# Kernel optimization log

Measured on AMD Instinct MI355X. Metric: run time of the kernel, lower is better.

Reference implementation:

```python
import jax, jax.numpy as jnp
import numpy as np

N_HEAD = 16
L_PARAM = 2  # module's L; min block = 2**L


def _build_sets(T, Lp):
    sets = []
    L = 2 ** Lp
    while L <= T:
        for i in range(T // L):
            sets.append((i * L, (i + 1) * L - 1))
        L *= 2
    return np.asarray(sets, dtype=np.int32)  # [nsets, 2]


def _get_slice(x_cum, l_idx, r_idx):
    # x_cum: [B, nh, T, hs]; returns cumulative-sum slice sums for each (l, r)
    r = x_cum[:, :, r_idx, :]
    l = x_cum[:, :, l_idx - 1, :] * (l_idx >= 1)[None, None, :, None]
    return r - l


def setup_inputs() -> dict:
    key = jax.random.key(0)
    k1, k2, k3 = jax.random.split(key, 3)
    B, T, C = 2, 2048, 1024
    x = jax.random.normal(k1, (B, T, C), dtype=jnp.float32)
    W_attn = jax.random.normal(k2, (3 * C, C), dtype=jnp.float32) * 0.02
    W_proj = jax.random.normal(k3, (C, C), dtype=jnp.float32) * 0.02
    return {"x": x, "W_attn": W_attn, "W_proj": W_proj}


def reference(x, W_attn, W_proj):
    B, T, C = x.shape
    nh, hs = N_HEAD, C // N_HEAD
    scale = 1.0 / np.sqrt(hs).astype(np.float32)

    qkv = x @ W_attn.T  # [B, T, 3C]
    q, k, v = jnp.split(qkv, 3, axis=2)
    q = q.reshape(B, T, nh, hs).transpose(0, 2, 1, 3)  # [B, nh, T, hs]
    k = k.reshape(B, T, nh, hs).transpose(0, 2, 1, 3)
    v = v.reshape(B, T, nh, hs).transpose(0, 2, 1, 3)

    # phi is identity, so q_phi = q, k_phi = k
    k_cum = jnp.cumsum(k, axis=2)
    v_cum = jnp.cumsum(v, axis=2)

    sets = _build_sets(T, L_PARAM)  # static, [nsets, 2]
    l_idx = jnp.asarray(sets[:, 0])
    r_idx = jnp.asarray(sets[:, 1])

    K = _get_slice(k_cum, l_idx, r_idx)  # [B, nh, nsets, hs]
    V = _get_slice(v_cum, l_idx, r_idx)

    t = jnp.arange(T)
    mask = t[:, None] >= r_idx[None, :]  # [T, nsets]

    att_logits = jnp.einsum('bhtd,bhsd->bhts', q, K) * scale
    att_logits = jnp.where(mask[None, None], att_logits, -jnp.inf)

    # tail term: remaining t % 2**L + 1 keys for each query
    Lmin = 2 ** L_PARAM
    tail_len = t % Lmin + 1
    l_tail = t - tail_len + 1
    K_tail = _get_slice(k_cum, l_tail, t)  # [B, nh, T, hs]
    V_tail = _get_slice(v_cum, l_tail, t)
    att_tail = jnp.sum(q * K_tail, axis=-1) * scale  # [B, nh, T]

    logits = jnp.concatenate([att_logits, att_tail[..., None]], axis=-1)
    att = jax.nn.softmax(logits, axis=-1)

    out = jnp.einsum('bhts,bhsd->bhtd', att[..., :-1], V) + att[..., -1:] * V_tail
    out = out.transpose(0, 2, 1, 3).reshape(B, T, C)
    return out @ W_proj.T
```

## Files before the change

### kernel.cpp

```cpp
#include <hip/hip_runtime.h>

typedef _Float16 f16x8 __attribute__((ext_vector_type(8)));
typedef unsigned short u16x8 __attribute__((ext_vector_type(8)));
typedef float f32x4  __attribute__((ext_vector_type(4)));
typedef unsigned short u16;

#define T_SEQ 2048
#define C_DIM 1024
#define NH 16
#define HS 64
#define S_SETS 1023
#define S_PAD 1024
#define SCALE 0.125f
#define NEG_BIG -1e30f

#define GLB(p) ((const __attribute__((address_space(1))) void*)(p))
#define LDS(p) ((__attribute__((address_space(3))) void*)(p))

__device__ __forceinline__ u16 f2h(float f) {
    _Float16 h = (_Float16)f;
    return __builtin_bit_cast(unsigned short, h);
}
__device__ __forceinline__ float h2f(u16 u) {
    _Float16 h = __builtin_bit_cast(_Float16, u);
    return (float)h;
}
__device__ __forceinline__ f32x4 mfmah(f16x8 a, f16x8 b, f32x4 c) {
    return __builtin_amdgcn_mfma_f32_16x16x32_f16(a, b, c, 0, 0, 0);
}

__global__ __launch_bounds__(256) void conv_f16(const float* __restrict__ in,
                                                u16* __restrict__ out, int n4) {
    int i = blockIdx.x * 256 + threadIdx.x;
    if (i >= n4) return;
    float4 f = ((const float4*)in)[i];
    ushort4 o;
    o.x = f2h(f.x); o.y = f2h(f.y); o.z = f2h(f.z); o.w = f2h(f.w);
    ((ushort4*)out)[i] = o;
}

__global__ __launch_bounds__(256) void gemm_qkv16(const u16* __restrict__ x16,
                                                  const u16* __restrict__ wa16,
                                                  u16* __restrict__ q16,
                                                  u16* __restrict__ k16,
                                                  u16* __restrict__ v16) {
    __shared__ u16 As[128 * 32];
    __shared__ u16 Bs[128 * 32];
    int tid = threadIdx.x, wv = tid >> 6, lane = tid & 63;
    int lm = lane & 15, quad = lane >> 4;
    int mt = blockIdx.x / 24, nt = blockIdx.x % 24;
    int wm = wv >> 1, wn = wv & 1;
    int m_off = wm * 64, n_off = wn * 64;

    const u16* gsrc;
    u16* ldst;
    int half = wv & 1;
    if (wv < 2) { gsrc = x16  + (size_t)(mt * 128 + half * 64) * C_DIM; ldst = As + half * 64 * 32; }
    else        { gsrc = wa16 + (size_t)(nt * 128 + half * 64) * C_DIM; ldst = Bs + half * 64 * 32; }
    int srow = lane >> 2, scol = (lane & 3) * 8;

    f32x4 acc[4][4];
    #pragma unroll
    for (int i = 0; i < 4; ++i)
        #pragma unroll
        for (int j = 0; j < 4; ++j) acc[i][j] = (f32x4){0.f, 0.f, 0.f, 0.f};

    for (int k0 = 0; k0 < C_DIM; k0 += 32) {
        __syncthreads();
        #pragma unroll
        for (int i = 0; i < 4; ++i) {
            int row = i * 16 + srow;
            __builtin_amdgcn_global_load_lds(
                GLB(gsrc + (size_t)row * C_DIM + k0 + scol),
                LDS(ldst + i * 512), 16, 0, 0);
        }
        __syncthreads();
        f16x8 af[4], bf[4];
        #pragma unroll
        for (int i = 0; i < 4; ++i) {
            af[i] = *(const f16x8*)(As + (m_off + i * 16 + lm) * 32 + quad * 8);
            bf[i] = *(const f16x8*)(Bs + (n_off + i * 16 + lm) * 32 + quad * 8);
        }
        #pragma unroll
        for (int mi = 0; mi < 4; ++mi)
            #pragma unroll
            for (int ni = 0; ni < 4; ++ni)
                acc[mi][ni] = mfmah(af[mi], bf[ni], acc[mi][ni]);
    }

    #pragma unroll
    for (int mi = 0; mi < 4; ++mi)
        #pragma unroll
        for (int ni = 0; ni < 4; ++ni) {
            int n = nt * 128 + n_off + ni * 16 + lm;
            int which = n >> 10, h = (n >> 6) & 15, d = n & 63;
            #pragma unroll
            for (int reg = 0; reg < 4; ++reg) {
                int m = mt * 128 + m_off + mi * 16 + quad * 4 + reg;
                int b_ = m >> 11, t = m & 2047;
                size_t oi = (((size_t)(b_ * NH + h)) * T_SEQ + t) * HS + d;
                float val = acc[mi][ni][reg];
                if (which == 0)      q16[oi] = f2h(val * SCALE);
                else if (which == 1) k16[oi] = f2h(val);
                else                 v16[oi] = f2h(val);
            }
        }
}

__global__ __launch_bounds__(256) void set_sums(const u16* __restrict__ k16,
                                                const u16* __restrict__ v16,
                                                u16* __restrict__ K16,
                                                u16* __restrict__ VT16) {
    int bh  = blockIdx.x;
    int src = blockIdx.y >> 2;
    int dc  = blockIdx.y & 3;
    int tid = threadIdx.x;
    __shared__ float lv0[512 * 16];
    __shared__ float lv1[256 * 16];
    const u16* sp = src ? v16 : k16;
    u16* op = src ? VT16 : K16;
    int dbase = dc * 16;
    for (int idx = tid; idx < 512 * 16; idx += 256) {
        int sg = idx >> 4, dd = idx & 15, d = dbase + dd;
        const u16* p = sp + ((size_t)bh * T_SEQ + sg * 4) * HS + d;
        float s = h2f(p[0]) + h2f(p[HS]) + h2f(p[2 * HS]) + h2f(p[3 * HS]);
        lv0[sg * 16 + dd] = s;
        size_t o = src ? ((size_t)bh * HS + d) * S_PAD + sg
                       : ((size_t)bh * S_PAD + sg) * HS + d;
        op[o] = f2h(s);
    }
    __syncthreads();
    int nsets = 256, offset = 512, lvl = 1;
    while (nsets >= 1) {
        float* sbuf = (lvl & 1) ? lv0 : lv1;
        float* dbuf = (lvl & 1) ? lv1 : lv0;
        for (int idx = tid; idx < nsets * 16; idx += 256) {
            int i = idx >> 4, dd = idx & 15, d = dbase + dd;
            float s = sbuf[(2 * i) * 16 + dd] + sbuf[(2 * i + 1) * 16 + dd];
            dbuf[i * 16 + dd] = s;
            int so = offset + i;
            size_t o = src ? ((size_t)bh * HS + d) * S_PAD + so
                           : ((size_t)bh * S_PAD + so) * HS + d;
            op[o] = f2h(s);
        }
        __syncthreads();
        offset += nsets; nsets >>= 1; lvl++;
    }
}

__global__ __launch_bounds__(256) void attn_flash16(const u16* __restrict__ q16,
                                                    const u16* __restrict__ k16,
                                                    const u16* __restrict__ v16,
                                                    const u16* __restrict__ K16,
                                                    const u16* __restrict__ VT16,
                                                    u16* __restrict__ att16) {
    int bh = blockIdx.y;
    int tid = threadIdx.x, wv = tid >> 6, lane = tid & 63;
    int lm = lane & 15, quad = lane >> 4;
    int tgrp = (wv < 2) ? (32 * blockIdx.x) : (2016 - 32 * blockIdx.x);
    int t0w = tgrp + (wv & 1) * 16;
    int twmax = t0w + 15;

    __shared__ u16 Ks[128 * 64];
    __shared__ u16 Pbuf[4][16 * 136];
    __shared__ float ptl[4][16];

    const u16* qg = q16 + ((size_t)bh * T_SEQ + t0w + lm) * HS;
    f16x8 a0 = *(const f16x8*)(qg + quad * 8);
    f16x8 a1 = *(const f16x8*)(qg + 32 + quad * 8);

    f32x4 O[4];
    #pragma unroll
    for (int i = 0; i < 4; ++i) O[i] = (f32x4){0.f, 0.f, 0.f, 0.f};
    f32x4 mrun = (f32x4){NEG_BIG, NEG_BIG, NEG_BIG, NEG_BIG};
    f32x4 lrun = (f32x4){0.f, 0.f, 0.f, 0.f};

    u16* Pw = &Pbuf[wv][0];
    const u16* vb = VT16 + (size_t)bh * HS * S_PAD;

    for (int c = 0; c < 8; ++c) {
        int s0 = c * 128;
        __syncthreads();
        {
            int row = tid >> 1, gb = (tid & 1) * 4, rx = row & 7;
            const u16* gk = K16 + ((size_t)bh * S_PAD + s0 + row) * HS;
            u16* dst = Ks + row * 64;
            #pragma unroll
            for (int uu = 0; uu < 4; ++uu) {
                int g = gb + uu;
                *(u16x8*)(dst + ((g ^ rx) << 3)) = *(const u16x8*)(gk + g * 8);
            }
        }
        __syncthreads();

        unsigned flags = 0;
        f32x4 lt[8];
        #pragma unroll
        for (int st = 0; st < 8; ++st) {
            int s = s0 + st * 16 + lm;
            bool sval = (s < S_SETS);
            int r = 0;
            if (sval) {
                int e = S_SETS - s;
                int l = __clz(e) - 22;
                int i0 = s - (1024 - (1024 >> l));
                r = (i0 + 1) * (4 << l) - 1;
            }
            unsigned long long bal = __ballot(sval && (r <= twmax));
            if (bal) {
                flags |= 1u << st;
                int sl = st * 16 + lm, sx = sl & 7;
                f16x8 b0 = *(const f16x8*)(Ks + sl * 64 + ((quad ^ sx) << 3));
                f16x8 b1 = *(const f16x8*)(Ks + sl * 64 + (((4 + quad) ^ sx) << 3));
                f32x4 a = (f32x4){0.f, 0.f, 0.f, 0.f};
                a = mfmah(a0, b0, a);
                a = mfmah(a1, b1, a);
                #pragma unroll
                for (int reg = 0; reg < 4; ++reg) {
                    int t = t0w + quad * 4 + reg;
                    lt[st][reg] = (sval && t >= r) ? a[reg] : NEG_BIG;
                }
            }
        }
        if (!flags) continue;

        f32x4 mc = (f32x4){NEG_BIG, NEG_BIG, NEG_BIG, NEG_BIG};
        #pragma unroll
        for (int st = 0; st < 8; ++st)
            if ((flags >> st) & 1u)
                #pragma unroll
                for (int reg = 0; reg < 4; ++reg) mc[reg] = fmaxf(mc[reg], lt[st][reg]);
        #pragma unroll
        for (int off = 1; off < 16; off <<= 1)
            #pragma unroll
            for (int reg = 0; reg < 4; ++reg)
                mc[reg] = fmaxf(mc[reg], __shfl_xor(mc[reg], off));
        f32x4 mnew, alpha, rs = (f32x4){0.f, 0.f, 0.f, 0.f};
        #pragma unroll
        for (int reg = 0; reg < 4; ++reg) {
            mnew[reg] = fmaxf(mrun[reg], mc[reg]);
            alpha[reg] = __expf(mrun[reg] - mnew[reg]);
        }
        #pragma unroll
        for (int st = 0; st < 8; ++st) {
            if ((flags >> st) & 1u) {
                #pragma unroll
                for (int reg = 0; reg < 4; ++reg) {
                    float lv = lt[st][reg];
                    float p = (lv > -5e29f) ? __expf(lv - mnew[reg]) : 0.f;
                    rs[reg] += p;
                    Pw[(quad * 4 + reg) * 136 + st * 16 + lm] = f2h(p);
                }
            } else {
                #pragma unroll
                for (int reg = 0; reg < 4; ++reg)
                    Pw[(quad * 4 + reg) * 136 + st * 16 + lm] = 0;
            }
        }
        #pragma unroll
        for (int off = 1; off < 16; off <<= 1)
            #pragma unroll
            for (int reg = 0; reg < 4; ++reg) rs[reg] += __shfl_xor(rs[reg], off);
        #pragma unroll
        for (int reg = 0; reg < 4; ++reg) {
            lrun[reg] = lrun[reg] * alpha[reg] + rs[reg];
            mrun[reg] = mnew[reg];
        }
        #pragma unroll
        for (int dt = 0; dt < 4; ++dt)
            #pragma unroll
            for (int reg = 0; reg < 4; ++reg) O[dt][reg] *= alpha[reg];

        #pragma unroll
        for (int kc = 0; kc < 4; ++kc) {
            if (!((flags >> (2 * kc)) & 3u)) continue;
            f16x8 afr = *(const f16x8*)(Pw + lm * 136 + kc * 32 + quad * 8);
            #pragma unroll
            for (int dt = 0; dt < 4; ++dt) {
                size_t vo = (size_t)(dt * 16 + lm) * S_PAD + s0 + kc * 32 + quad * 8;
                f16x8 bv = *(const f16x8*)(vb + vo);
                O[dt] = mfmah(afr, bv, O[dt]);
            }
        }
    }

    {
        int rqr = lane >> 2, prt = lane & 3;
        int tt = t0w + rqr;
        int lenr = (tt & 3) + 1;
        float ktv[16];
        #pragma unroll
        for (int dd = 0; dd < 16; ++dd) ktv[dd] = 0.f;
        for (int j = 0; j < lenr; ++j) {
            const u16* kp = k16 + ((size_t)bh * T_SEQ + tt - j) * HS + prt * 16;
            #pragma unroll
            for (int dd = 0; dd < 16; ++dd) ktv[dd] += h2f(kp[dd]);
        }
        const u16* tq = q16 + ((size_t)bh * T_SEQ + tt) * HS + prt * 16;
        float tlp = 0.f;
        #pragma unroll
        for (int dd = 0; dd < 16; ++dd) tlp += h2f(tq[dd]) * ktv[dd];
        tlp += __shfl_xor(tlp, 1);
        tlp += __shfl_xor(tlp, 2);
        if (prt == 0) ptl[wv][rqr] = tlp;
    }
    __syncthreads();

    int b_ = bh >> 4, h_ = bh & 15;
    #pragma unroll
    for (int reg = 0; reg < 4; ++reg) {
        int row = quad * 4 + reg;
        int t = t0w + row;
        float tl = ptl[wv][row];
        float mfin = fmaxf(mrun[reg], tl);
        float pt = __expf(tl - mfin);
        float af = __expf(mrun[reg] - mfin);
        float inv = 1.0f / (lrun[reg] * af + pt);
        int len = (t & 3) + 1;
        #pragma unroll
        for (int dt = 0; dt < 4; ++dt) {
            int d = dt * 16 + lm;
            const u16* vp = v16 + ((size_t)bh * T_SEQ + t) * HS + d;
            float vt = 0.f;
            for (int j = 0; j < len; ++j) vt += h2f(vp[-(j * HS)]);
            float val = (O[dt][reg] * af + pt * vt) * inv;
            att16[((size_t)(b_ * T_SEQ + t)) * C_DIM + h_ * HS + d] = f2h(val);
        }
    }
}

__global__ __launch_bounds__(256) void gemm_proj16(const u16* __restrict__ a_,
                                                   const u16* __restrict__ w,
                                                   float* __restrict__ out) {
    __shared__ u16 As[128 * 32];
    __shared__ u16 Bs[128 * 32];
    int tid = threadIdx.x, wv = tid >> 6, lane = tid & 63;
    int lm = lane & 15, quad = lane >> 4;
    int mt = blockIdx.x >> 3, nt = blockIdx.x & 7;
    int wm = wv >> 1, wn = wv & 1;
    int m_off = wm * 64, n_off = wn * 64;

    const u16* gsrc;
    u16* ldst;
    int half = wv & 1;
    if (wv < 2) { gsrc = a_ + (size_t)(mt * 128 + half * 64) * C_DIM; ldst = As + half * 64 * 32; }
    else        { gsrc = w  + (size_t)(nt * 128 + half * 64) * C_DIM; ldst = Bs + half * 64 * 32; }
    int srow = lane >> 2, scol = (lane & 3) * 8;

    f32x4 acc[4][4];
    #pragma unroll
    for (int i = 0; i < 4; ++i)
        #pragma unroll
        for (int j = 0; j < 4; ++j) acc[i][j] = (f32x4){0.f, 0.f, 0.f, 0.f};

    for (int k0 = 0; k0 < C_DIM; k0 += 32) {
        __syncthreads();
        #pragma unroll
        for (int i = 0; i < 4; ++i) {
            int row = i * 16 + srow;
            __builtin_amdgcn_global_load_lds(
                GLB(gsrc + (size_t)row * C_DIM + k0 + scol),
                LDS(ldst + i * 512), 16, 0, 0);
        }
        __syncthreads();
        f16x8 af[4], bf[4];
        #pragma unroll
        for (int i = 0; i < 4; ++i) {
            af[i] = *(const f16x8*)(As + (m_off + i * 16 + lm) * 32 + quad * 8);
            bf[i] = *(const f16x8*)(Bs + (n_off + i * 16 + lm) * 32 + quad * 8);
        }
        #pragma unroll
        for (int mi = 0; mi < 4; ++mi)
            #pragma unroll
            for (int ni = 0; ni < 4; ++ni)
                acc[mi][ni] = mfmah(af[mi], bf[ni], acc[mi][ni]);
    }

    #pragma unroll
    for (int mi = 0; mi < 4; ++mi)
        #pragma unroll
        for (int ni = 0; ni < 4; ++ni) {
            int n = nt * 128 + n_off + ni * 16 + lm;
            #pragma unroll
            for (int reg = 0; reg < 4; ++reg) {
                int m = mt * 128 + m_off + mi * 16 + quad * 4 + reg;
                out[(size_t)m * C_DIM + n] = acc[mi][ni][reg];
            }
        }
}

extern "C" void kernel_launch(void* const* d_in, const int* in_sizes, int n_in,
                              void* d_out, int out_size, void* d_ws, size_t ws_size,
                              hipStream_t stream) {
    const float* x     = (const float*)d_in[0];
    const float* Wattn = (const float*)d_in[1];
    const float* Wproj = (const float*)d_in[2];
    float* out = (float*)d_out;
    char* ws = (char*)d_ws;
    u16* x16   = (u16*)(ws + 0);
    u16* wa16  = (u16*)(ws + 8388608);
    u16* wp16  = (u16*)(ws + 14680064);
    u16* q16   = (u16*)(ws + 16777216);
    u16* k16   = (u16*)(ws + 25165824);
    u16* v16   = (u16*)(ws + 33554432);
    u16* K16   = (u16*)(ws + 41943040);
    u16* VT16  = (u16*)(ws + 46137344);
    u16* att16 = (u16*)(ws + 50331648);

    hipLaunchKernelGGL(conv_f16, dim3(4096), dim3(256), 0, stream, x, x16, 1048576);
    hipLaunchKernelGGL(conv_f16, dim3(3072), dim3(256), 0, stream, Wattn, wa16, 786432);
    hipLaunchKernelGGL(conv_f16, dim3(1024), dim3(256), 0, stream, Wproj, wp16, 262144);
    hipLaunchKernelGGL(gemm_qkv16, dim3(768), dim3(256), 0, stream, x16, wa16, q16, k16, v16);
    hipLaunchKernelGGL(set_sums, dim3(32, 8), dim3(256), 0, stream, k16, v16, K16, VT16);
    hipLaunchKernelGGL(attn_flash16, dim3(32, 32), dim3(256), 0, stream,
                       q16, k16, v16, K16, VT16, att16);
    hipLaunchKernelGGL(gemm_proj16, dim3(256), dim3(256), 0, stream, att16, wp16, out);
}
```

Before: 236.3 us.

## Sort set sums by right endpoint so attention visits only valid set chunks

A new kernel computes a permutation that orders the block sets by their right index r, and set_sums writes K and V^T in that sorted order. The attention kernel then loops only over the chunks that can hold valid sets for its query tile and stops early once a chunk is partly masked. Query tiles are regrouped so all four waves in a block cover 64 contiguous rows, which replaces the old pairing of early and late rows. This removes wasted chunk loads and MFMA work on fully masked sets, but it drops the old balancing of work across blocks and adds a tiny extra launch plus scattered writes.

```diff
diff --git a/kernel.cpp b/kernel.cpp
--- a/kernel.cpp
+++ b/kernel.cpp
@@ -13,6 +13,7 @@
 #define S_PAD 1024
 #define SCALE 0.125f
 #define NEG_BIG -1e30f
+#define M_INIT -1e20f
 
 #define GLB(p) ((const __attribute__((address_space(1))) void*)(p))
 #define LDS(p) ((__attribute__((address_space(3))) void*)(p))
@@ -27,6 +28,28 @@
 }
 __device__ __forceinline__ f32x4 mfmah(f16x8 a, f16x8 b, f32x4 c) {
     return __builtin_amdgcn_mfma_f32_16x16x32_f16(a, b, c, 0, 0, 0);
+}
+
+__global__ __launch_bounds__(256) void build_perm(int* __restrict__ rankArr,
+                                                  int* __restrict__ r32) {
+    int s = blockIdx.x * 256 + threadIdx.x;
+    if (s >= 1024) return;
+    if (s == 1023) { r32[1023] = 0x7fffffff; return; }
+    int e = S_SETS - s;
+    int l = __clz(e) - 22;
+    int base = 1024 - (1024 >> l);
+    int i = s - base;
+    int L = 4 << l;
+    int r = (i + 1) * L - 1;
+    int rank = l;
+    #pragma unroll
+    for (int j = 0; j < 10; ++j) {
+        int cnt = r >> (j + 2);
+        int cap = 512 >> j;
+        rank += (cnt < cap) ? cnt : cap;
+    }
+    rankArr[s] = rank;
+    r32[rank] = r;
 }
 
 __global__ __launch_bounds__(256) void conv_f16(const float* __restrict__ in,
@@ -109,6 +132,7 @@
 
 __global__ __launch_bounds__(256) void set_sums(const u16* __restrict__ k16,
                                                 const u16* __restrict__ v16,
+                                                const int* __restrict__ rankArr,
                                                 u16* __restrict__ K16,
                                                 u16* __restrict__ VT16) {
     int bh  = blockIdx.x;
@@ -125,8 +149,9 @@
         const u16* p = sp + ((size_t)bh * T_SEQ + sg * 4) * HS + d;
         float s = h2f(p[0]) + h2f(p[HS]) + h2f(p[2 * HS]) + h2f(p[3 * HS]);
         lv0[sg * 16 + dd] = s;
-        size_t o = src ? ((size_t)bh * HS + d) * S_PAD + sg
-                       : ((size_t)bh * S_PAD + sg) * HS + d;
+        int rnk = rankArr[sg];
+        size_t o = src ? ((size_t)bh * HS + d) * S_PAD + rnk
+                       : ((size_t)bh * S_PAD + rnk) * HS + d;
         op[o] = f2h(s);
     }
     __syncthreads();
@@ -138,13 +163,18 @@
             int i = idx >> 4, dd = idx & 15, d = dbase + dd;
             float s = sbuf[(2 * i) * 16 + dd] + sbuf[(2 * i + 1) * 16 + dd];
             dbuf[i * 16 + dd] = s;
-            int so = offset + i;
-            size_t o = src ? ((size_t)bh * HS + d) * S_PAD + so
-                           : ((size_t)bh * S_PAD + so) * HS + d;
+            int rnk = rankArr[offset + i];
+            size_t o = src ? ((size_t)bh * HS + d) * S_PAD + rnk
+                           : ((size_t)bh * S_PAD + rnk) * HS + d;
             op[o] = f2h(s);
         }
         __syncthreads();
         offset += nsets; nsets >>= 1; lvl++;
+    }
+    if (tid < 16) {
+        int d = dbase + tid;
+        if (src == 0) K16[((size_t)bh * S_PAD + 1023) * HS + d] = 0;
+        else          VT16[((size_t)bh * HS + d) * S_PAD + 1023] = 0;
     }
 }
 
@@ -153,18 +183,28 @@
                                                     const u16* __restrict__ v16,
                                                     const u16* __restrict__ K16,
                                                     const u16* __restrict__ VT16,
+                                                    const int* __restrict__ r32g,
                                                     u16* __restrict__ att16) {
     int bh = blockIdx.y;
+    int t0 = 1984 - 64 * blockIdx.x;
     int tid = threadIdx.x, wv = tid >> 6, lane = tid & 63;
     int lm = lane & 15, quad = lane >> 4;
-    int tgrp = (wv < 2) ? (32 * blockIdx.x) : (2016 - 32 * blockIdx.x);
-    int t0w = tgrp + (wv & 1) * 16;
+    int t0w = t0 + wv * 16;
     int twmax = t0w + 15;
 
     __shared__ u16 Ks[128 * 64];
     __shared__ u16 Pbuf[4][16 * 136];
     __shared__ float ptl[4][16];
 
+    int nch;
+    {
+        int tp1 = t0 + 64;
+        int nval = 0;
+        #pragma unroll
+        for (int j = 2; j <= 11; ++j) nval += tp1 >> j;
+        nch = (nval + 127) >> 7;
+    }
+
     const u16* qg = q16 + ((size_t)bh * T_SEQ + t0w + lm) * HS;
     f16x8 a0 = *(const f16x8*)(qg + quad * 8);
     f16x8 a1 = *(const f16x8*)(qg + 32 + quad * 8);
@@ -172,13 +212,14 @@
     f32x4 O[4];
     #pragma unroll
     for (int i = 0; i < 4; ++i) O[i] = (f32x4){0.f, 0.f, 0.f, 0.f};
-    f32x4 mrun = (f32x4){NEG_BIG, NEG_BIG, NEG_BIG, NEG_BIG};
+    f32x4 mrun = (f32x4){M_INIT, M_INIT, M_INIT, M_INIT};
     f32x4 lrun = (f32x4){0.f, 0.f, 0.f, 0.f};
 
     u16* Pw = &Pbuf[wv][0];
     const u16* vb = VT16 + (size_t)bh * HS * S_PAD;
-
-    for (int c = 0; c < 8; ++c) {
+    bool done = false;
+
+    for (int c = 0; c < nch; ++c) {
         int s0 = c * 128;
         __syncthreads();
         {
@@ -192,21 +233,15 @@
             }
         }
         __syncthreads();
+        if (done) continue;
 
         unsigned flags = 0;
         f32x4 lt[8];
         #pragma unroll
         for (int st = 0; st < 8; ++st) {
             int s = s0 + st * 16 + lm;
-            bool sval = (s < S_SETS);
-            int r = 0;
-            if (sval) {
-                int e = S_SETS - s;
-                int l = __clz(e) - 22;
-                int i0 = s - (1024 - (1024 >> l));
-                r = (i0 + 1) * (4 << l) - 1;
-            }
-            unsigned long long bal = __ballot(sval && (r <= twmax));
+            int r = r32g[s];
+            unsigned long long bal = __ballot(r <= twmax);
             if (bal) {
                 flags |= 1u << st;
                 int sl = st * 16 + lm, sx = sl & 7;
@@ -218,11 +253,11 @@
                 #pragma unroll
                 for (int reg = 0; reg < 4; ++reg) {
                     int t = t0w + quad * 4 + reg;
-                    lt[st][reg] = (sval && t >= r) ? a[reg] : NEG_BIG;
+                    lt[st][reg] = (r <= t) ? a[reg] : NEG_BIG;
                 }
             }
         }
-        if (!flags) continue;
+        if (!flags) { done = true; continue; }
 
         f32x4 mc = (f32x4){NEG_BIG, NEG_BIG, NEG_BIG, NEG_BIG};
         #pragma unroll
@@ -246,8 +281,7 @@
             if ((flags >> st) & 1u) {
                 #pragma unroll
                 for (int reg = 0; reg < 4; ++reg) {
-                    float lv = lt[st][reg];
-                    float p = (lv > -5e29f) ? __expf(lv - mnew[reg]) : 0.f;
+                    float p = __expf(lt[st][reg] - mnew[reg]);
                     rs[reg] += p;
                     Pw[(quad * 4 + reg) * 136 + st * 16 + lm] = f2h(p);
                 }
@@ -282,6 +316,7 @@
                 O[dt] = mfmah(afr, bv, O[dt]);
             }
         }
+        if (flags != 0xFFu) done = true;
     }
 
     {
@@ -406,13 +441,16 @@
     u16* K16   = (u16*)(ws + 41943040);
     u16* VT16  = (u16*)(ws + 46137344);
     u16* att16 = (u16*)(ws + 50331648);
-
+    int* rankA = (int*)(ws + 58720256);
+    int* r32   = (int*)(ws + 58724352);
+
+    hipLaunchKernelGGL(build_perm, dim3(4), dim3(256), 0, stream, rankA, r32);
     hipLaunchKernelGGL(conv_f16, dim3(4096), dim3(256), 0, stream, x, x16, 1048576);
     hipLaunchKernelGGL(conv_f16, dim3(3072), dim3(256), 0, stream, Wattn, wa16, 786432);
     hipLaunchKernelGGL(conv_f16, dim3(1024), dim3(256), 0, stream, Wproj, wp16, 262144);
     hipLaunchKernelGGL(gemm_qkv16, dim3(768), dim3(256), 0, stream, x16, wa16, q16, k16, v16);
-    hipLaunchKernelGGL(set_sums, dim3(32, 8), dim3(256), 0, stream, k16, v16, K16, VT16);
+    hipLaunchKernelGGL(set_sums, dim3(32, 8), dim3(256), 0, stream, k16, v16, rankA, K16, VT16);
     hipLaunchKernelGGL(attn_flash16, dim3(32, 32), dim3(256), 0, stream,
-                       q16, k16, v16, K16, VT16, att16);
+                       q16, k16, v16, K16, VT16, r32, att16);
     hipLaunchKernelGGL(gemm_proj16, dim3(256), dim3(256), 0, stream, att16, wp16, out);
 }
```

After: 282.4 us. +19.5%, slower.
